# Optimization experiments

Hardware: AMD Instinct MI355X
Metric: run time of the kernel (lower is better)

## Reference

```python
import jax, jax.numpy as jnp
import numpy as np

EMBED = 1024
HEADS = 16
HEAD_DIM = EMBED // HEADS


def setup_inputs() -> dict:
    key = jax.random.key(0)
    ks = jax.random.split(key, 9)
    s = 0.02
    return {
        "hidden_states": jax.random.normal(ks[0], (1, 4, 1500, EMBED), dtype=jnp.float32),
        "q_w": jax.random.normal(ks[1], (EMBED, EMBED), dtype=jnp.float32) * s,
        "q_b": jax.random.normal(ks[2], (EMBED,), dtype=jnp.float32) * s,
        "k_w": jax.random.normal(ks[3], (EMBED, EMBED), dtype=jnp.float32) * s,
        "v_w": jax.random.normal(ks[4], (EMBED, EMBED), dtype=jnp.float32) * s,
        "v_b": jax.random.normal(ks[5], (EMBED,), dtype=jnp.float32) * s,
        "out_w": jax.random.normal(ks[6], (EMBED, EMBED), dtype=jnp.float32) * s,
        "out_b": jax.random.normal(ks[7], (EMBED,), dtype=jnp.float32) * s,
    }


def reference(hidden_states, q_w, q_b, k_w, v_w, v_b, out_w, out_b):
    # hidden_states: [1, B, S, E]
    _, bsz, tgt_len, _ = hidden_states.shape
    x = hidden_states[0]  # [B, S, E]
    scaling = HEAD_DIM ** -0.5

    def split_heads(t):  # [B, S, E] -> [B, H, S, Dh]
        return t.reshape(bsz, tgt_len, HEADS, HEAD_DIM).transpose(0, 2, 1, 3)

    # Linear layers use torch convention: y = x @ W.T + b  (k_proj has no bias)
    q = split_heads((x @ q_w.T + q_b) * scaling)
    k = split_heads(x @ k_w.T)
    v = split_heads(x @ v_w.T + v_b)

    # attention scores [B, H, S, S]
    attn_weights = jnp.einsum("bhqd,bhkd->bhqk", q, k)
    attn_probs = jax.nn.softmax(attn_weights, axis=-1)
    attn_out = jnp.einsum("bhqk,bhkd->bhqd", attn_probs, v)  # [B, H, S, Dh]

    attn_out = attn_out.transpose(0, 2, 1, 3).reshape(1, bsz, tgt_len, EMBED)
    return attn_out @ out_w.T + out_b
```

## Files before the change

### kernel.cpp

```cpp
#include <hip/hip_runtime.h>
#include <cstddef>
#include <cstdint>

#define EMB 1024
#define SEQ 1500
#define NB 4
#define NH 16
#define DH 64
#define MTOT (NB*SEQ)
#define VTS 1536

typedef __bf16 bf16;
typedef __bf16 bf16x4 __attribute__((ext_vector_type(4)));
typedef __bf16 bf16x8 __attribute__((ext_vector_type(8)));
typedef short  s16x4  __attribute__((ext_vector_type(4)));
typedef float  f32x4  __attribute__((ext_vector_type(4)));

#define LOG2E 1.44269504088896340736f

__device__ __forceinline__ void async16(const void* g, const void* l) {
    __builtin_amdgcn_global_load_lds(
        (const __attribute__((address_space(1))) uint32_t*)g,
        (__attribute__((address_space(3))) uint32_t*)l, 16, 0, 0);
}

__device__ __forceinline__ uint32_t pack_bf16_trunc(float e0, float e1) {
    return __builtin_amdgcn_perm(__builtin_bit_cast(uint32_t, e1),
                                 __builtin_bit_cast(uint32_t, e0), 0x07060302u);
}

struct CvtArgs {
    const float* xs; bf16* xd;
    const float* w[4]; bf16* wd[4];
};

__global__ __launch_bounds__(256) void cvt_kernel(CvtArgs a) {
    const size_t NX = (size_t)MTOT * EMB;
    const size_t NW = (size_t)EMB * EMB;
    const size_t tot = NX + 4 * NW;
    for (size_t i = ((size_t)blockIdx.x * 256 + threadIdx.x) * 4; i < tot;
         i += (size_t)gridDim.x * 1024) {
        const float* s; bf16* d; size_t off;
        if (i < NX) { s = a.xs; d = a.xd; off = i; }
        else {
            size_t j = i - NX;
            int wi = (int)(j >> 20);
            off = j & (NW - 1);
            s = a.w[wi]; d = a.wd[wi];
        }
        float4 v = *(const float4*)(s + off);
        bf16x4 o = { (bf16)v.x, (bf16)v.y, (bf16)v.z, (bf16)v.w };
        *(bf16x4*)(d + off) = o;
    }
}

__global__ __launch_bounds__(256) void gemm_fused(
    const bf16* __restrict__ X,
    const bf16* __restrict__ W0, const bf16* __restrict__ W1, const bf16* __restrict__ W2,
    const float* __restrict__ b_q, const float* __restrict__ b_v,
    bf16* __restrict__ Oq, bf16* __restrict__ Ok, bf16* __restrict__ Ovt,
    int M)
{
    __shared__ bf16 As[2][128 * 32];
    __shared__ bf16 Bs[2][128 * 32];
    const int tid = threadIdx.x;
    const int lane = tid & 63, w = tid >> 6;
    const int q = lane >> 4, lr = lane & 15;
    const int wr = w >> 1, wc = w & 1;

    const int id = blockIdx.x;
    const int t_ = id >> 3;
    const int mtile = (id & 7) + (t_ % 6) * 8;
    const int y = t_ / 6;
    const int m0 = mtile * 128;
    const int proj = y >> 3;
    const int n0 = (y & 7) * 128;

    const bf16 *PA, *PB;
    int baseA, baseB, limA, limB;
    if (proj == 2) {
        PA = X;  baseA = m0; limA = M;
        PB = W2; baseB = n0; limB = EMB;
    } else {
        PA = (proj == 0) ? W0 : W1;
        baseA = n0; limA = EMB;
        PB = X; baseB = m0; limB = M;
    }

    f32x4 acc[4][4] = {};

    const int srow = w * 32 + (lane >> 2);
    const int swz_ch = (((lane & 3) ^ ((lane >> 3) & 3))) * 8;
    const bf16* pA[2]; const bf16* pB[2];
#pragma unroll
    for (int i = 0; i < 2; i++) {
        int ra = baseA + srow + i * 16; ra = ra < limA ? ra : limA - 1;
        int rb = baseB + srow + i * 16; rb = rb < limB ? rb : limB - 1;
        pA[i] = PA + (size_t)ra * EMB + swz_ch;
        pB[i] = PB + (size_t)rb * EMB + swz_ch;
    }

#pragma unroll
    for (int i = 0; i < 2; i++) {
        async16(pA[i], As[0] + (w * 2 + i) * 512);
        async16(pB[i], Bs[0] + (w * 2 + i) * 512);
    }

    const int qsw = (q ^ ((lr >> 1) & 3)) * 8;
    const int arow = (wr * 64 + lr) * 32;
    const int brow = (wc * 64 + lr) * 32;

    for (int k0 = 0; k0 < EMB; k0 += 32) {
        const int cur = (k0 >> 5) & 1;
        __syncthreads();
        const int nxt = k0 + 32;
        if (nxt < EMB) {
#pragma unroll
            for (int i = 0; i < 2; i++) {
                async16(pA[i] + nxt, As[cur ^ 1] + (w * 2 + i) * 512);
                async16(pB[i] + nxt, Bs[cur ^ 1] + (w * 2 + i) * 512);
            }
        }
        const bf16* Ab = As[cur];
        const bf16* Bb = Bs[cur];
        bf16x8 af[4], bfr[4];
#pragma unroll
        for (int t = 0; t < 4; t++) {
            af[t]  = *(const bf16x8*)(Ab + arow + t * 512 + qsw);
            bfr[t] = *(const bf16x8*)(Bb + brow + t * 512 + qsw);
        }
#pragma unroll
        for (int ti = 0; ti < 4; ti++)
#pragma unroll
            for (int tj = 0; tj < 4; tj++)
                acc[ti][tj] = __builtin_amdgcn_mfma_f32_16x16x32_bf16(
                    af[ti], bfr[tj], acc[ti][tj], 0, 0, 0);
    }

    if (proj <= 1) {
        const float scale = (proj == 0) ? 0.125f * LOG2E : 1.0f;
        const float* bias = (proj == 0) ? b_q : nullptr;
        bf16* O = (proj == 0) ? Oq : Ok;
#pragma unroll
        for (int tj = 0; tj < 4; tj++) {
            const int m = m0 + wc * 64 + tj * 16 + lr;
            if (m >= M) continue;
            const int b_ = m / SEQ, s_ = m % SEQ;
#pragma unroll
            for (int ti = 0; ti < 4; ti++) {
                const int nb = n0 + wr * 64 + ti * 16 + q * 4;
                const int h = nb >> 6, d = nb & 63;
                float4 b4 = bias ? *(const float4*)(bias + nb)
                                 : make_float4(0.f, 0.f, 0.f, 0.f);
                bf16x4 o;
                o[0] = (bf16)((acc[ti][tj][0] + b4.x) * scale);
                o[1] = (bf16)((acc[ti][tj][1] + b4.y) * scale);
                o[2] = (bf16)((acc[ti][tj][2] + b4.z) * scale);
                o[3] = (bf16)((acc[ti][tj][3] + b4.w) * scale);
                *(bf16x4*)(O + (((size_t)b_ * NH + h) * SEQ + s_) * DH + d) = o;
            }
        }
    } else {
#pragma unroll
        for (int ti = 0; ti < 4; ti++) {
            const int mb = m0 + wr * 64 + ti * 16 + q * 4;
            if (mb >= M) continue;
            const int b_ = mb / SEQ, s_ = mb % SEQ;
#pragma unroll
            for (int tj = 0; tj < 4; tj++) {
                const int nb = n0 + wc * 64 + tj * 16 + lr;
                const int h = nb >> 6, d = nb & 63;
                const float bv = b_v[nb];
                bf16x4 o;
                o[0] = (bf16)(acc[ti][tj][0] + bv);
                o[1] = (bf16)(acc[ti][tj][1] + bv);
                o[2] = (bf16)(acc[ti][tj][2] + bv);
                o[3] = (bf16)(acc[ti][tj][3] + bv);
                *(bf16x4*)(Ovt + ((size_t)(b_ * NH + h) * DH + d) * VTS + s_) = o;
            }
        }
    }
}

__global__ __launch_bounds__(256) void gemm_out(
    const bf16* __restrict__ X, const bf16* __restrict__ Wo,
    const float* __restrict__ b_o, float* __restrict__ Of, int M)
{
    __shared__ bf16 As[2][128 * 32];
    __shared__ bf16 Bs[2][128 * 32];
    const int tid = threadIdx.x;
    const int lane = tid & 63, w = tid >> 6;
    const int q = lane >> 4, lr = lane & 15;
    const int wr = w >> 1, wc = w & 1;

    const int id = blockIdx.x;
    const int mtile = (id & 7) + ((id >> 3) % 6) * 8;
    const int ntile = (id >> 3) / 6;
    const int m0 = mtile * 128, n0 = ntile * 128;

    const int srow = w * 32 + (lane >> 2);
    const int swz_ch = (((lane & 3) ^ ((lane >> 3) & 3))) * 8;
    const bf16* pA[2]; const bf16* pB[2];
#pragma unroll
    for (int i = 0; i < 2; i++) {
        int ra = n0 + srow + i * 16;
        int rb = m0 + srow + i * 16; rb = rb < M ? rb : M - 1;
        pA[i] = Wo + (size_t)ra * EMB + swz_ch;
        pB[i] = X + (size_t)rb * EMB + swz_ch;
    }

#pragma unroll
    for (int i = 0; i < 2; i++) {
        async16(pA[i], As[0] + (w * 2 + i) * 512);
        async16(pB[i], Bs[0] + (w * 2 + i) * 512);
    }

    f32x4 acc[4][4] = {};
    const int qsw = (q ^ ((lr >> 1) & 3)) * 8;
    const int arow = (wr * 64 + lr) * 32;
    const int brow = (wc * 64 + lr) * 32;

    for (int k0 = 0; k0 < EMB; k0 += 32) {
        const int cur = (k0 >> 5) & 1;
        __syncthreads();
        const int nxt = k0 + 32;
        if (nxt < EMB) {
#pragma unroll
            for (int i = 0; i < 2; i++) {
                async16(pA[i] + nxt, As[cur ^ 1] + (w * 2 + i) * 512);
                async16(pB[i] + nxt, Bs[cur ^ 1] + (w * 2 + i) * 512);
            }
        }
        bf16x8 af[4], bfr[4];
#pragma unroll
        for (int t = 0; t < 4; t++) {
            af[t]  = *(const bf16x8*)(As[cur] + arow + t * 512 + qsw);
            bfr[t] = *(const bf16x8*)(Bs[cur] + brow + t * 512 + qsw);
        }
#pragma unroll
        for (int ti = 0; ti < 4; ti++)
#pragma unroll
            for (int tj = 0; tj < 4; tj++)
                acc[ti][tj] = __builtin_amdgcn_mfma_f32_16x16x32_bf16(
                    af[ti], bfr[tj], acc[ti][tj], 0, 0, 0);
    }

#pragma unroll
    for (int tj = 0; tj < 4; tj++) {
        const int m = m0 + wc * 64 + tj * 16 + lr;
        if (m >= M) continue;
#pragma unroll
        for (int ti = 0; ti < 4; ti++) {
            const int nb = n0 + wr * 64 + ti * 16 + q * 4;
            const float4 b4 = *(const float4*)(b_o + nb);
            float4 o;
            o.x = acc[ti][tj][0] + b4.x;
            o.y = acc[ti][tj][1] + b4.y;
            o.z = acc[ti][tj][2] + b4.z;
            o.w = acc[ti][tj][3] + b4.w;
            *(float4*)(Of + (size_t)m * EMB + nb) = o;
        }
    }
}

#define QG 3
__global__ __launch_bounds__(256) void attn_mfma(
    const bf16* __restrict__ Qb, const bf16* __restrict__ Kb,
    const bf16* __restrict__ Vt, bf16* __restrict__ ctx)
{
    __shared__ bf16 Ks[2][64 * 64];
    __shared__ bf16 Vs[2][64 * 64];
    const int tid = threadIdx.x;
    const int lane = tid & 63, w = tid >> 6;
    const int q = lane >> 4, lr = lane & 15;
    const int bh = blockIdx.x, b_ = bh >> 4, h_ = bh & 15;
    const int q0 = blockIdx.y * (QG * 64);
    const size_t base = (size_t)bh * SEQ * DH;
    const size_t vbase = (size_t)bh * DH * VTS;

    int qrow[QG];
    bf16x8 qf[QG][2];
#pragma unroll
    for (int g = 0; g < QG; g++) {
        qrow[g] = q0 + g * 64 + w * 16 + lr;
        const int qrc = qrow[g] < SEQ ? qrow[g] : (SEQ - 1);
        qf[g][0] = *(const bf16x8*)(Qb + base + (size_t)qrc * DH + q * 8);
        qf[g][1] = *(const bf16x8*)(Qb + base + (size_t)qrc * DH + 32 + q * 8);
    }

    f32x4 oacc[QG][4] = {};
    f32x4 lacc[QG] = {};
    const s16x4 ones = { (short)0x3F80, (short)0x3F80, (short)0x3F80, (short)0x3F80 };

    const int srow = tid >> 3;
    const int sch8 = ((tid & 7) ^ (srow & 7)) * 8;
    const int kswz = lr & 7;

    const int NT = (SEQ + 63) / 64;

    {
        int r0 = srow, r1 = srow + 32;
        async16(Kb + base + (size_t)r0 * DH + sch8, Ks[0] + tid * 8);
        async16(Kb + base + (size_t)r1 * DH + sch8, Ks[0] + tid * 8 + 2048);
        async16(Vt + vbase + (size_t)srow * VTS + sch8,        Vs[0] + tid * 8);
        async16(Vt + vbase + (size_t)(srow + 32) * VTS + sch8, Vs[0] + tid * 8 + 2048);
    }

    for (int kt = 0; kt < NT; kt++) {
        const int k0 = kt * 64;
        const int cur = kt & 1;
        __syncthreads();

        if (kt + 1 < NT) {
            const int kn = k0 + 64;
            int r0 = kn + srow;      if (r0 >= SEQ) r0 = SEQ - 1;
            int r1 = kn + srow + 32; if (r1 >= SEQ) r1 = SEQ - 1;
            async16(Kb + base + (size_t)r0 * DH + sch8, Ks[cur ^ 1] + tid * 8);
            async16(Kb + base + (size_t)r1 * DH + sch8, Ks[cur ^ 1] + tid * 8 + 2048);
            async16(Vt + vbase + (size_t)srow * VTS + kn + sch8,
                    Vs[cur ^ 1] + tid * 8);
            async16(Vt + vbase + (size_t)(srow + 32) * VTS + kn + sch8,
                    Vs[cur ^ 1] + tid * 8 + 2048);
        }

        const bf16* Kc = Ks[cur];
        const bf16* Vc = Vs[cur];

        bf16x8 kf[2][4];
#pragma unroll
        for (int s = 0; s < 2; s++)
#pragma unroll
            for (int mt = 0; mt < 4; mt++)
                kf[s][mt] = *(const bf16x8*)(Kc + (mt * 16 + lr) * 64 +
                                             ((4 * s + q) ^ kswz) * 8);

        s16x4 pf[QG][4];
#pragma unroll
        for (int g = 0; g < QG; g++) {
            f32x4 st[4] = {};
#pragma unroll
            for (int s = 0; s < 2; s++)
#pragma unroll
                for (int mt = 0; mt < 4; mt++)
                    st[mt] = __builtin_amdgcn_mfma_f32_16x16x32_bf16(
                        kf[s][mt], qf[g][s], st[mt], 0, 0, 0);

            if (k0 + 64 > SEQ) {
#pragma unroll
                for (int mt = 0; mt < 4; mt++)
#pragma unroll
                    for (int r = 0; r < 4; r++)
                        if (k0 + mt * 16 + q * 4 + r >= SEQ) st[mt][r] = -16384.0f;
            }

#pragma unroll
            for (int mt = 0; mt < 4; mt++) {
                float e0 = __builtin_amdgcn_exp2f(st[mt][0]);
                float e1 = __builtin_amdgcn_exp2f(st[mt][1]);
                float e2 = __builtin_amdgcn_exp2f(st[mt][2]);
                float e3 = __builtin_amdgcn_exp2f(st[mt][3]);
                uint32_t lo = pack_bf16_trunc(e0, e1);
                uint32_t hi = pack_bf16_trunc(e2, e3);
                uint2 pk = { lo, hi };
                pf[g][mt] = __builtin_bit_cast(s16x4, pk);
            }
#pragma unroll
            for (int c = 0; c < 4; c++)
                lacc[g] = __builtin_amdgcn_mfma_f32_16x16x16bf16_1k(
                    ones, pf[g][c], lacc[g], 0, 0, 0);
        }

#pragma unroll
        for (int c = 0; c < 4; c++) {
#pragma unroll
            for (int dt = 0; dt < 4; dt++) {
                const s16x4 vf = __builtin_bit_cast(s16x4,
                    *(const bf16x4*)(Vc + (dt * 16 + lr) * 64 +
                                     ((2 * c + (q >> 1)) ^ kswz) * 8 + (q & 1) * 4));
#pragma unroll
                for (int g = 0; g < QG; g++)
                    oacc[g][dt] = __builtin_amdgcn_mfma_f32_16x16x16bf16_1k(
                        vf, pf[g][c], oacc[g][dt], 0, 0, 0);
            }
        }
    }

#pragma unroll
    for (int g = 0; g < QG; g++) {
        const float inv = 1.0f / lacc[g][0];
        if (qrow[g] < SEQ) {
            const size_t rowoff = ((size_t)b_ * SEQ + qrow[g]) * EMB + h_ * DH;
#pragma unroll
            for (int dt = 0; dt < 4; dt++) {
                bf16x4 o;
#pragma unroll
                for (int r = 0; r < 4; r++) o[r] = (bf16)(oacc[g][dt][r] * inv);
                *(bf16x4*)(ctx + rowoff + dt * 16 + q * 4) = o;
            }
        }
    }
}

extern "C" void kernel_launch(void* const* d_in, const int* in_sizes, int n_in,
                              void* d_out, int out_size, void* d_ws, size_t ws_size,
                              hipStream_t stream) {
    const float* x     = (const float*)d_in[0];
    const float* q_w   = (const float*)d_in[1];
    const float* q_b   = (const float*)d_in[2];
    const float* k_w   = (const float*)d_in[3];
    const float* v_w   = (const float*)d_in[4];
    const float* v_b   = (const float*)d_in[5];
    const float* out_w = (const float*)d_in[6];
    const float* out_b = (const float*)d_in[7];
    float* out = (float*)d_out;

    const size_t nbuf = (size_t)MTOT * EMB;
    const size_t nvt  = (size_t)NB * NH * DH * VTS;
    const size_t nw   = (size_t)EMB * EMB;
    bf16* xb  = (bf16*)d_ws;
    bf16* qws = xb  + nbuf;
    bf16* kws = qws + nbuf;
    bf16* vtw = kws + nbuf;
    bf16* wqb = vtw + nvt;
    bf16* wkb = wqb + nw;
    bf16* wvb = wkb + nw;
    bf16* wob = wvb + nw;
    bf16* ctx = xb;

    CvtArgs ca;
    ca.xs = x;      ca.xd = xb;
    ca.w[0] = q_w;  ca.wd[0] = wqb;
    ca.w[1] = k_w;  ca.wd[1] = wkb;
    ca.w[2] = v_w;  ca.wd[2] = wvb;
    ca.w[3] = out_w; ca.wd[3] = wob;
    cvt_kernel<<<dim3(2560), 256, 0, stream>>>(ca);

    gemm_fused<<<dim3(48 * 24), 256, 0, stream>>>(
        xb, wqb, wkb, wvb, q_b, v_b, qws, kws, vtw, MTOT);

    attn_mfma<<<dim3(NB * NH, (SEQ + QG * 64 - 1) / (QG * 64)), 256, 0, stream>>>(
        qws, kws, vtw, ctx);

    gemm_out<<<dim3(384), 256, 0, stream>>>(ctx, wob, out_b, out, MTOT);
}
```

Before: 239.7 us.

## Compute Q and K projections in one block sharing the X tile

Q and K projection tiles are now computed by the same block: each block stages one X tile and two weight tiles, then accumulates two output sets. V blocks stay separate, so the grid shrinks from 1152 to 768 blocks. The aim is to halve X loads and LDS staging for Q/K. In exchange the Q/K blocks use twice the accumulator registers, which brings register pressure and a launch_bounds hint of 3 waves, and the load between the Q/K blocks and the V blocks is uneven. The K weights are addressed as a fixed offset from the Q weights, which relies on the workspace buffers being contiguous.

```diff
diff --git a/kernel.cpp b/kernel.cpp
--- a/kernel.cpp
+++ b/kernel.cpp
@@ -54,58 +54,60 @@
     }
 }
 
-__global__ __launch_bounds__(256) void gemm_fused(
+__global__ __launch_bounds__(256, 3) void gemm_fused(
     const bf16* __restrict__ X,
     const bf16* __restrict__ W0, const bf16* __restrict__ W1, const bf16* __restrict__ W2,
     const float* __restrict__ b_q, const float* __restrict__ b_v,
     bf16* __restrict__ Oq, bf16* __restrict__ Ok, bf16* __restrict__ Ovt,
     int M)
 {
-    __shared__ bf16 As[2][128 * 32];
-    __shared__ bf16 Bs[2][128 * 32];
+    __shared__ bf16 A0s[2][128 * 32];
+    __shared__ bf16 A1s[2][128 * 32];
+    __shared__ bf16 Bs [2][128 * 32];
     const int tid = threadIdx.x;
     const int lane = tid & 63, w = tid >> 6;
     const int q = lane >> 4, lr = lane & 15;
     const int wr = w >> 1, wc = w & 1;
 
     const int id = blockIdx.x;
-    const int t_ = id >> 3;
-    const int mtile = (id & 7) + (t_ % 6) * 8;
-    const int y = t_ / 6;
-    const int m0 = mtile * 128;
-    const int proj = y >> 3;
-    const int n0 = (y & 7) * 128;
-
-    const bf16 *PA, *PB;
-    int baseA, baseB, limA, limB;
-    if (proj == 2) {
-        PA = X;  baseA = m0; limA = M;
-        PB = W2; baseB = n0; limB = EMB;
-    } else {
-        PA = (proj == 0) ? W0 : W1;
-        baseA = n0; limA = EMB;
-        PB = X; baseB = m0; limB = M;
-    }
-
-    f32x4 acc[4][4] = {};
+    const bool isV = id >= 384;
+    const int vid = isV ? id - 384 : id;
+    const int mtile = (vid & 7) + ((vid >> 3) % 6) * 8;
+    const int ntile = (vid >> 3) / 6;
+    const int m0 = mtile * 128, n0 = ntile * 128;
 
     const int srow = w * 32 + (lane >> 2);
     const int swz_ch = (((lane & 3) ^ ((lane >> 3) & 3))) * 8;
-    const bf16* pA[2]; const bf16* pB[2];
+
+    const bf16* pA0[2]; const bf16* pB[2];
+    const size_t WOFF = (size_t)(W1 - W0);
 #pragma unroll
     for (int i = 0; i < 2; i++) {
-        int ra = baseA + srow + i * 16; ra = ra < limA ? ra : limA - 1;
-        int rb = baseB + srow + i * 16; rb = rb < limB ? rb : limB - 1;
-        pA[i] = PA + (size_t)ra * EMB + swz_ch;
-        pB[i] = PB + (size_t)rb * EMB + swz_ch;
-    }
-
-#pragma unroll
-    for (int i = 0; i < 2; i++) {
-        async16(pA[i], As[0] + (w * 2 + i) * 512);
-        async16(pB[i], Bs[0] + (w * 2 + i) * 512);
-    }
-
+        int mr = m0 + srow + i * 16; mr = mr < M ? mr : M - 1;
+        int nr = n0 + srow + i * 16;
+        if (!isV) {
+            pA0[i] = W0 + (size_t)nr * EMB + swz_ch;
+            pB[i]  = X  + (size_t)mr * EMB + swz_ch;
+        } else {
+            pA0[i] = X  + (size_t)mr * EMB + swz_ch;
+            pB[i]  = W2 + (size_t)nr * EMB + swz_ch;
+        }
+    }
+
+#define STAGE(buf, off) do { \
+    async16(pA0[0] + (off), A0s[buf] + (w * 2 + 0) * 512); \
+    async16(pA0[1] + (off), A0s[buf] + (w * 2 + 1) * 512); \
+    async16(pB[0]  + (off), Bs[buf]  + (w * 2 + 0) * 512); \
+    async16(pB[1]  + (off), Bs[buf]  + (w * 2 + 1) * 512); \
+    if (!isV) { \
+        async16(pA0[0] + WOFF + (off), A1s[buf] + (w * 2 + 0) * 512); \
+        async16(pA0[1] + WOFF + (off), A1s[buf] + (w * 2 + 1) * 512); } \
+    } while (0)
+
+    STAGE(0, 0);
+
+    f32x4 acc0[4][4] = {};
+    f32x4 acc1[4][4] = {};
     const int qsw = (q ^ ((lr >> 1) & 3)) * 8;
     const int arow = (wr * 64 + lr) * 32;
     const int brow = (wc * 64 + lr) * 32;
@@ -114,33 +116,36 @@
         const int cur = (k0 >> 5) & 1;
         __syncthreads();
         const int nxt = k0 + 32;
-        if (nxt < EMB) {
-#pragma unroll
-            for (int i = 0; i < 2; i++) {
-                async16(pA[i] + nxt, As[cur ^ 1] + (w * 2 + i) * 512);
-                async16(pB[i] + nxt, Bs[cur ^ 1] + (w * 2 + i) * 512);
-            }
-        }
-        const bf16* Ab = As[cur];
-        const bf16* Bb = Bs[cur];
+        if (nxt < EMB) STAGE(cur ^ 1, nxt);
+
         bf16x8 af[4], bfr[4];
 #pragma unroll
         for (int t = 0; t < 4; t++) {
-            af[t]  = *(const bf16x8*)(Ab + arow + t * 512 + qsw);
-            bfr[t] = *(const bf16x8*)(Bb + brow + t * 512 + qsw);
+            bfr[t] = *(const bf16x8*)(Bs[cur]  + brow + t * 512 + qsw);
+            af[t]  = *(const bf16x8*)(A0s[cur] + arow + t * 512 + qsw);
         }
 #pragma unroll
         for (int ti = 0; ti < 4; ti++)
 #pragma unroll
             for (int tj = 0; tj < 4; tj++)
-                acc[ti][tj] = __builtin_amdgcn_mfma_f32_16x16x32_bf16(
-                    af[ti], bfr[tj], acc[ti][tj], 0, 0, 0);
-    }
-
-    if (proj <= 1) {
-        const float scale = (proj == 0) ? 0.125f * LOG2E : 1.0f;
-        const float* bias = (proj == 0) ? b_q : nullptr;
-        bf16* O = (proj == 0) ? Oq : Ok;
+                acc0[ti][tj] = __builtin_amdgcn_mfma_f32_16x16x32_bf16(
+                    af[ti], bfr[tj], acc0[ti][tj], 0, 0, 0);
+        if (!isV) {
+#pragma unroll
+            for (int t = 0; t < 4; t++)
+                af[t] = *(const bf16x8*)(A1s[cur] + arow + t * 512 + qsw);
+#pragma unroll
+            for (int ti = 0; ti < 4; ti++)
+#pragma unroll
+                for (int tj = 0; tj < 4; tj++)
+                    acc1[ti][tj] = __builtin_amdgcn_mfma_f32_16x16x32_bf16(
+                        af[ti], bfr[tj], acc1[ti][tj], 0, 0, 0);
+        }
+    }
+#undef STAGE
+
+    if (!isV) {
+        const float scale = 0.125f * LOG2E;
 #pragma unroll
         for (int tj = 0; tj < 4; tj++) {
             const int m = m0 + wc * 64 + tj * 16 + lr;
@@ -150,14 +155,19 @@
             for (int ti = 0; ti < 4; ti++) {
                 const int nb = n0 + wr * 64 + ti * 16 + q * 4;
                 const int h = nb >> 6, d = nb & 63;
-                float4 b4 = bias ? *(const float4*)(bias + nb)
-                                 : make_float4(0.f, 0.f, 0.f, 0.f);
-                bf16x4 o;
-                o[0] = (bf16)((acc[ti][tj][0] + b4.x) * scale);
-                o[1] = (bf16)((acc[ti][tj][1] + b4.y) * scale);
-                o[2] = (bf16)((acc[ti][tj][2] + b4.z) * scale);
-                o[3] = (bf16)((acc[ti][tj][3] + b4.w) * scale);
-                *(bf16x4*)(O + (((size_t)b_ * NH + h) * SEQ + s_) * DH + d) = o;
+                const size_t ooff = (((size_t)b_ * NH + h) * SEQ + s_) * DH + d;
+                const float4 b4 = *(const float4*)(b_q + nb);
+                bf16x4 oq, ok;
+                oq[0] = (bf16)((acc0[ti][tj][0] + b4.x) * scale);
+                oq[1] = (bf16)((acc0[ti][tj][1] + b4.y) * scale);
+                oq[2] = (bf16)((acc0[ti][tj][2] + b4.z) * scale);
+                oq[3] = (bf16)((acc0[ti][tj][3] + b4.w) * scale);
+                ok[0] = (bf16)(acc1[ti][tj][0]);
+                ok[1] = (bf16)(acc1[ti][tj][1]);
+                ok[2] = (bf16)(acc1[ti][tj][2]);
+                ok[3] = (bf16)(acc1[ti][tj][3]);
+                *(bf16x4*)(Oq + ooff) = oq;
+                *(bf16x4*)(Ok + ooff) = ok;
             }
         }
     } else {
@@ -172,10 +182,10 @@
                 const int h = nb >> 6, d = nb & 63;
                 const float bv = b_v[nb];
                 bf16x4 o;
-                o[0] = (bf16)(acc[ti][tj][0] + bv);
-                o[1] = (bf16)(acc[ti][tj][1] + bv);
-                o[2] = (bf16)(acc[ti][tj][2] + bv);
-                o[3] = (bf16)(acc[ti][tj][3] + bv);
+                o[0] = (bf16)(acc0[ti][tj][0] + bv);
+                o[1] = (bf16)(acc0[ti][tj][1] + bv);
+                o[2] = (bf16)(acc0[ti][tj][2] + bv);
+                o[3] = (bf16)(acc0[ti][tj][3] + bv);
                 *(bf16x4*)(Ovt + ((size_t)(b_ * NH + h) * DH + d) * VTS + s_) = o;
             }
         }
@@ -435,7 +445,7 @@
     ca.w[3] = out_w; ca.wd[3] = wob;
     cvt_kernel<<<dim3(2560), 256, 0, stream>>>(ca);
 
-    gemm_fused<<<dim3(48 * 24), 256, 0, stream>>>(
+    gemm_fused<<<dim3(768), 256, 0, stream>>>(
         xb, wqb, wkb, wvb, q_b, v_b, qws, kws, vtw, MTOT);
 
     attn_mfma<<<dim3(NB * NH, (SEQ + QG * 64 - 1) / (QG * 64)), 256, 0, stream>>>(
```

Result: faster. 231.1 us (median of 3 runs) (-3.6%).
